# Kernel tuning notes

Measured on AMD Instinct MI355X. Metric: run time of the kernel, lower is better.

## Reference

```python
import jax, jax.numpy as jnp
import numpy as np

N_CHANNELS = 1024
N_HEADS = 16
BLOCK_SIZE = 2048
BATCH = 4
SEQ = 2048


def setup_inputs() -> dict:
    key = jax.random.key(0)
    k_x, k_wqkv, k_wproj = jax.random.split(key, 3)
    x = jax.random.normal(k_x, (BATCH, SEQ, N_CHANNELS), dtype=jnp.float32)
    # torch nn.Linear: y = x @ W.T + b, W shape [out, in], init normal(std=0.02)
    W_qkv = jax.random.normal(k_wqkv, (3 * N_CHANNELS, N_CHANNELS), dtype=jnp.float32) * 0.02
    b_qkv = jnp.zeros((3 * N_CHANNELS,), dtype=jnp.float32)
    W_proj = jax.random.normal(k_wproj, (N_CHANNELS, N_CHANNELS), dtype=jnp.float32) * 0.02
    b_proj = jnp.zeros((N_CHANNELS,), dtype=jnp.float32)
    return {"x": x, "W_qkv": W_qkv, "b_qkv": b_qkv, "W_proj": W_proj, "b_proj": b_proj}


def reference(x, W_qkv, b_qkv, W_proj, b_proj):
    bs, n, n_channels = x.shape
    n_heads = N_HEADS
    head_dim = n_channels // n_heads
    scale = head_dim ** (-0.5)

    qkv = x @ W_qkv.T + b_qkv                              # [b, n, 3C]
    qkv = qkv.reshape(bs, n, 3, n_heads, head_dim)
    q, k, v = qkv[:, :, 0], qkv[:, :, 1], qkv[:, :, 2]     # [b, n, h, d]

    logits = jnp.einsum('bthc,bshc->bhts', q, k) * scale   # [b, h, t, s]
    # causal mask: log(tril(ones)) = 0 below diagonal, -inf above
    causal = jnp.tril(jnp.ones((n, n), dtype=bool))
    logits = jnp.where(causal[None, None], logits, -jnp.inf)
    attn = jax.nn.softmax(logits, axis=-1)

    output = jnp.einsum('bhts,bshc->bthc', attn, v)        # [b, t, h, d]
    output = output.reshape(bs, n, n_channels)
    output = output @ W_proj.T + b_proj
    return output
```

## Files before the change

kernel.cpp:

```cpp
#include <hip/hip_runtime.h>
#include <hip/hip_bf16.h>
#include <stdint.h>

#define BATCH 4
#define SEQ   2048
#define NC    1024
#define NH    16
#define HD    64
#define NT    16

typedef __bf16 bf16x8 __attribute__((ext_vector_type(8)));
typedef __bf16 bf16x2 __attribute__((ext_vector_type(2)));
typedef float  f32x4  __attribute__((ext_vector_type(4)));
typedef float  f32x16 __attribute__((ext_vector_type(16)));

#define DEV __device__ __forceinline__

DEV unsigned short f2bf(float f) {
    union { float f; unsigned u; } v; v.f = f;
    unsigned r = (v.u + 0x7fffu + ((v.u >> 16) & 1u)) >> 16;
    return (unsigned short)r;
}

DEV float fast_exp2(float x) {
#if __has_builtin(__builtin_amdgcn_exp2f)
    return __builtin_amdgcn_exp2f(x);
#else
    return exp2f(x);
#endif
}

DEV void plane32_swap(uint32_t& a, uint32_t& b) {
#if __has_builtin(__builtin_amdgcn_permlane32_swap)
    auto r = __builtin_amdgcn_permlane32_swap(a, b, false, false);
    a = (uint32_t)r[0];
    b = (uint32_t)r[1];
#else
    uint32_t sa = __shfl_xor(a, 32), sb = __shfl_xor(b, 32);
    const bool hi = ((threadIdx.x & 63) >= 32);
    uint32_t na = hi ? sb : a;
    uint32_t nb = hi ? b : sa;
    a = na; b = nb;
#endif
}

#define GLDS16(gsrc, ldst)                                                           \
    __builtin_amdgcn_global_load_lds(                                                \
        (const __attribute__((address_space(1))) unsigned int*)(gsrc),               \
        (__attribute__((address_space(3))) unsigned int*)(ldst), 16, 0, 0)

#define CVT_N0 (BATCH * SEQ * NC / 4)
#define CVT_N1 (3 * NC * NC / 4)
#define CVT_N2 (NC * NC / 4)

__global__ void cvt_all_kernel(const float* __restrict__ x, unsigned short* __restrict__ xb,
                               const float* __restrict__ wq, unsigned short* __restrict__ wqb,
                               const float* __restrict__ wp, unsigned short* __restrict__ wpb) {
    int i = blockIdx.x * 256 + threadIdx.x;
    const float* src;
    unsigned short* dst;
    if (i < CVT_N0) {
        src = x; dst = xb;
    } else if (i < CVT_N0 + CVT_N1) {
        i -= CVT_N0; src = wq; dst = wqb;
    } else {
        i -= CVT_N0 + CVT_N1; src = wp; dst = wpb;
    }
    float4 v = reinterpret_cast<const float4*>(src)[i];
    ushort4 o;
    o.x = f2bf(v.x); o.y = f2bf(v.y); o.z = f2bf(v.z); o.w = f2bf(v.w);
    reinterpret_cast<ushort4*>(dst)[i] = o;
}

template <bool BF16_OUT>
__global__ __launch_bounds__(256, 2) void gemm_bt_kernel(
    const unsigned short* __restrict__ A,
    const unsigned short* __restrict__ W,
    const float* __restrict__ bias,
    void* __restrict__ Cout,
    int M, int N, int K, int scale_n, float scale)
{
    __shared__ __align__(16) char Alds[128 * 128];
    __shared__ __align__(16) char Blds[128 * 128];

    const int tid = threadIdx.x;
    const int w = tid >> 6, l = tid & 63, g = l >> 4, lr = l & 15;
    const int nt = N >> 7;
    const int cpx = gridDim.x >> 3;
    const int bid = (blockIdx.x & 7) * cpx + (blockIdx.x >> 3);
    const int mtile = bid / nt, ntile = bid % nt;
    const int m0 = mtile << 7, n0 = ntile << 7;
    const int wr = (w >> 1) << 6, wc = (w & 1) << 6;

    f32x4 acc[4][4] = {};

    for (int kt = 0; kt < K; kt += 64) {
        if (kt) __syncthreads();
#pragma unroll
        for (int i = 0; i < 4; ++i) {
            const int issue = (i << 2) + w;
            const int row = (issue << 3) + (l >> 3);
            const int chunk = (l & 7) ^ (row & 7);
            GLDS16((const char*)(A + (size_t)(m0 + row) * K + kt) + (chunk << 4),
                   Alds + (issue << 10));
        }
#pragma unroll
        for (int i = 0; i < 4; ++i) {
            const int issue = (i << 2) + w;
            const int row = (issue << 3) + (l >> 3);
            const int chunk = (l & 7) ^ (row & 7);
            GLDS16((const char*)(W + (size_t)(n0 + row) * K + kt) + (chunk << 4),
                   Blds + (issue << 10));
        }
        __syncthreads();

#pragma unroll
        for (int kb = 0; kb < 2; ++kb) {
            bf16x8 af[4], bfr[4];
#pragma unroll
            for (int mf = 0; mf < 4; ++mf) {
                const int row = wr + (mf << 4) + lr;
                const int chunk = ((kb << 2) + g) ^ (row & 7);
                af[mf] = *reinterpret_cast<const bf16x8*>(Alds + row * 128 + (chunk << 4));
            }
#pragma unroll
            for (int nf = 0; nf < 4; ++nf) {
                const int row = wc + (nf << 4) + lr;
                const int chunk = ((kb << 2) + g) ^ (row & 7);
                bfr[nf] = *reinterpret_cast<const bf16x8*>(Blds + row * 128 + (chunk << 4));
            }
#pragma unroll
            for (int mf = 0; mf < 4; ++mf)
#pragma unroll
                for (int nf = 0; nf < 4; ++nf)
                    acc[mf][nf] = __builtin_amdgcn_mfma_f32_16x16x32_bf16(
                        af[mf], bfr[nf], acc[mf][nf], 0, 0, 0);
        }
    }

#pragma unroll
    for (int mf = 0; mf < 4; ++mf) {
#pragma unroll
        for (int nf = 0; nf < 4; ++nf) {
            const int n = n0 + wc + (nf << 4) + lr;
            const float bscale = (n < scale_n) ? scale : 1.0f;
            const float bv = bias[n];
#pragma unroll
            for (int r = 0; r < 4; ++r) {
                const int m = m0 + wr + (mf << 4) + (g << 2) + r;
                float v2 = (acc[mf][nf][r] + bv) * bscale;
                if (BF16_OUT)
                    ((unsigned short*)Cout)[(size_t)m * N + n] = f2bf(v2);
                else
                    ((float*)Cout)[(size_t)m * N + n] = v2;
            }
        }
    }
}

__global__ __launch_bounds__(256, 2) void gemm_bt64_kernel(
    const unsigned short* __restrict__ A,
    const unsigned short* __restrict__ W,
    const float* __restrict__ bias,
    float* __restrict__ Cout,
    int M, int N, int K)
{
    __shared__ __align__(16) char Alds[64 * 128];
    __shared__ __align__(16) char Blds[128 * 128];

    const int tid = threadIdx.x;
    const int w = tid >> 6, l = tid & 63, g = l >> 4, lr = l & 15;
    const int nt = N >> 7;
    const int cpx = gridDim.x >> 3;
    const int bid = (blockIdx.x & 7) * cpx + (blockIdx.x >> 3);
    const int mtile = bid / nt, ntile = bid % nt;
    const int m0 = mtile << 6, n0 = ntile << 7;
    const int wr = (w >> 1) << 5, wc = (w & 1) << 6;

    f32x4 acc[2][4] = {};

    for (int kt = 0; kt < K; kt += 64) {
        if (kt) __syncthreads();
#pragma unroll
        for (int i = 0; i < 2; ++i) {
            const int issue = (i << 2) + w;
            const int row = (issue << 3) + (l >> 3);
            const int chunk = (l & 7) ^ (row & 7);
            GLDS16((const char*)(A + (size_t)(m0 + row) * K + kt) + (chunk << 4),
                   Alds + (issue << 10));
        }
#pragma unroll
        for (int i = 0; i < 4; ++i) {
            const int issue = (i << 2) + w;
            const int row = (issue << 3) + (l >> 3);
            const int chunk = (l & 7) ^ (row & 7);
            GLDS16((const char*)(W + (size_t)(n0 + row) * K + kt) + (chunk << 4),
                   Blds + (issue << 10));
        }
        __syncthreads();

#pragma unroll
        for (int kb = 0; kb < 2; ++kb) {
            bf16x8 af[2], bfr[4];
#pragma unroll
            for (int mf = 0; mf < 2; ++mf) {
                const int row = wr + (mf << 4) + lr;
                const int chunk = ((kb << 2) + g) ^ (row & 7);
                af[mf] = *reinterpret_cast<const bf16x8*>(Alds + row * 128 + (chunk << 4));
            }
#pragma unroll
            for (int nf = 0; nf < 4; ++nf) {
                const int row = wc + (nf << 4) + lr;
                const int chunk = ((kb << 2) + g) ^ (row & 7);
                bfr[nf] = *reinterpret_cast<const bf16x8*>(Blds + row * 128 + (chunk << 4));
            }
#pragma unroll
            for (int mf = 0; mf < 2; ++mf)
#pragma unroll
                for (int nf = 0; nf < 4; ++nf)
                    acc[mf][nf] = __builtin_amdgcn_mfma_f32_16x16x32_bf16(
                        af[mf], bfr[nf], acc[mf][nf], 0, 0, 0);
        }
    }

#pragma unroll
    for (int mf = 0; mf < 2; ++mf) {
#pragma unroll
        for (int nf = 0; nf < 4; ++nf) {
            const int n = n0 + wc + (nf << 4) + lr;
            const float bv = bias[n];
#pragma unroll
            for (int r = 0; r < 4; ++r) {
                const int m = m0 + wr + (mf << 4) + (g << 2) + r;
                Cout[(size_t)m * N + n] = acc[mf][nf][r] + bv;
            }
        }
    }
}

__global__ __launch_bounds__(256, 4) void attn_kernel(
    const unsigned short* __restrict__ qkv,
    unsigned short* __restrict__ ctx)
{
    __shared__ __align__(16) char Klds[2][8192];
    __shared__ __align__(16) char Vt[2][64 * 144];

    const int tid = threadIdx.x;
    const int w = tid >> 6, l = tid & 63, hi = l >> 5, lq = l & 31;
    const int bid = blockIdx.x;
    const int qt = NT - 1 - (bid >> 6);
    const int h = (bid >> 2) & 15, b = bid & 3;
    const unsigned short* base = qkv + (size_t)b * SEQ * 3072 + h * 64;

    const int vkey0 = (tid >> 5) << 3;
    const int vd0   = (tid & 31) << 1;
    const unsigned short* vbase = base + 2048 + (size_t)vkey0 * 3072 + vd0;

    const int q0 = (qt << 7) + (w << 5);
    const int q = q0 + lq;
    const int ntiles = (qt + 1) << 1;

    bf16x8 qfr[4];
#pragma unroll
    for (int ds = 0; ds < 4; ++ds)
        qfr[ds] = *reinterpret_cast<const bf16x8*>(
            base + (size_t)q * 3072 + (ds << 4) + (hi << 3));

    f32x16 acc0 = {}, acc1 = {};
    float lrun = 0.f;

    uint32_t vreg[8];

#pragma unroll
    for (int i = 0; i < 8; ++i)
        vreg[i] = *reinterpret_cast<const uint32_t*>(vbase + (size_t)i * 3072);
#pragma unroll
    for (int i = 0; i < 2; ++i) {
        const int issue = (i << 2) + w;
        const int row = (issue << 3) + (l >> 3);
        const int chunk = (l & 7) ^ (row & 7);
        GLDS16((const char*)(base + 1024 + (size_t)row * 3072) + (chunk << 4),
               Klds[0] + (issue << 10));
    }
    {
        uint4 a, bq;
        a.x = (vreg[0] & 0xffffu) | (vreg[1] << 16);
        a.y = (vreg[2] & 0xffffu) | (vreg[3] << 16);
        a.z = (vreg[4] & 0xffffu) | (vreg[5] << 16);
        a.w = (vreg[6] & 0xffffu) | (vreg[7] << 16);
        bq.x = (vreg[0] >> 16) | (vreg[1] & 0xffff0000u);
        bq.y = (vreg[2] >> 16) | (vreg[3] & 0xffff0000u);
        bq.z = (vreg[4] >> 16) | (vreg[5] & 0xffff0000u);
        bq.w = (vreg[6] >> 16) | (vreg[7] & 0xffff0000u);
        *reinterpret_cast<uint4*>(Vt[0] + vd0 * 144 + vkey0 * 2) = a;
        *reinterpret_cast<uint4*>(Vt[0] + (vd0 + 1) * 144 + vkey0 * 2) = bq;
    }
    __syncthreads();

    for (int t = 0; t < ntiles; ++t) {
        const int cur = t & 1;
        const int kv0 = t << 6;
        const bool pf_ = (t + 1 < ntiles);

        if (pf_) {
            const int kv1 = kv0 + 64;
#pragma unroll
            for (int i = 0; i < 8; ++i)
                vreg[i] = *reinterpret_cast<const uint32_t*>(
                    vbase + (size_t)(kv1 + i) * 3072);
#pragma unroll
            for (int i = 0; i < 2; ++i) {
                const int issue = (i << 2) + w;
                const int row = (issue << 3) + (l >> 3);
                const int chunk = (l & 7) ^ (row & 7);
                GLDS16((const char*)(base + 1024 + (size_t)(kv1 + row) * 3072) + (chunk << 4),
                       Klds[cur ^ 1] + (issue << 10));
            }
        }

        if (kv0 <= q0 + 31) {
            const bool do1 = (kv0 + 32 <= q0 + 31);

            f32x16 st0 = {}, st1 = {};
#pragma unroll
            for (int ds = 0; ds < 4; ++ds) {
                const int chunk = (((ds << 1) + hi) ^ (lq & 7)) << 4;
                bf16x8 k0 = *reinterpret_cast<const bf16x8*>(
                    Klds[cur] + lq * 128 + chunk);
                st0 = __builtin_amdgcn_mfma_f32_32x32x16_bf16(k0, qfr[ds], st0, 0, 0, 0);
            }
            if (do1) {
#pragma unroll
                for (int ds = 0; ds < 4; ++ds) {
                    const int chunk = (((ds << 1) + hi) ^ (lq & 7)) << 4;
                    bf16x8 k1 = *reinterpret_cast<const bf16x8*>(
                        Klds[cur] + (lq + 32) * 128 + chunk);
                    st1 = __builtin_amdgcn_mfma_f32_32x32x16_bf16(k1, qfr[ds], st1, 0, 0, 0);
                }
            }

            if (kv0 + 31 > q0) {
#pragma unroll
                for (int r = 0; r < 16; ++r) {
                    const int key = kv0 + ((r & 3) + ((r >> 2) << 3) + (hi << 2));
                    if (key > q) st0[r] = -INFINITY;
                }
            }
            if (do1 && kv0 + 63 > q0) {
#pragma unroll
                for (int r = 0; r < 16; ++r) {
                    const int key = kv0 + 32 + ((r & 3) + ((r >> 2) << 3) + (hi << 2));
                    if (key > q) st1[r] = -INFINITY;
                }
            }

            float rs = 0.f;
#pragma unroll
            for (int r = 0; r < 16; ++r) { st0[r] = fast_exp2(st0[r]); rs += st0[r]; }
            if (do1) {
#pragma unroll
                for (int r = 0; r < 16; ++r) { st1[r] = fast_exp2(st1[r]); rs += st1[r]; }
            }
            lrun += rs;

            uint32_t pk0[8], pk1[8];
#pragma unroll
            for (int sp = 0; sp < 4; ++sp)
#pragma unroll
                for (int c = 0; c < 2; ++c) {
                    bf16x2 t0 = {(__bf16)st0[(sp << 2) + (c << 1)],
                                 (__bf16)st0[(sp << 2) + (c << 1) + 1]};
                    pk0[(sp << 1) + c] = __builtin_bit_cast(uint32_t, t0);
                }
            if (do1) {
#pragma unroll
                for (int sp = 0; sp < 4; ++sp)
#pragma unroll
                    for (int c = 0; c < 2; ++c) {
                        bf16x2 t1 = {(__bf16)st1[(sp << 2) + (c << 1)],
                                     (__bf16)st1[(sp << 2) + (c << 1) + 1]};
                        pk1[(sp << 1) + c] = __builtin_bit_cast(uint32_t, t1);
                    }
            }

            const int nkt = do1 ? 4 : 2;
#pragma unroll
            for (int kt = 0; kt < 4; ++kt) {
                if (kt >= nkt) break;
                const int s0 = (kt & 1) << 1;
                uint32_t x0, x1, y0, y1;
                if (kt < 2) {
                    x0 = pk0[(s0 << 1) + 0]; x1 = pk0[(s0 << 1) + 1];
                    y0 = pk0[(s0 << 1) + 2]; y1 = pk0[(s0 << 1) + 3];
                } else {
                    x0 = pk1[(s0 << 1) + 0]; x1 = pk1[(s0 << 1) + 1];
                    y0 = pk1[(s0 << 1) + 2]; y1 = pk1[(s0 << 1) + 3];
                }
                plane32_swap(x0, y0);
                plane32_swap(x1, y1);
                union { uint32_t u[4]; bf16x8 v; } pf;
                pf.u[0] = x0; pf.u[1] = x1; pf.u[2] = y0; pf.u[3] = y1;

                const char* vrow = Vt[cur] + ((kt << 4) + (hi << 3)) * 2;
                bf16x8 vf0 = *reinterpret_cast<const bf16x8*>(vrow + lq * 144);
                bf16x8 vf1 = *reinterpret_cast<const bf16x8*>(vrow + (lq + 32) * 144);
                acc0 = __builtin_amdgcn_mfma_f32_32x32x16_bf16(vf0, pf.v, acc0, 0, 0, 0);
                acc1 = __builtin_amdgcn_mfma_f32_32x32x16_bf16(vf1, pf.v, acc1, 0, 0, 0);
            }
        }

        if (pf_) {
            uint4 a, bq;
            a.x = (vreg[0] & 0xffffu) | (vreg[1] << 16);
            a.y = (vreg[2] & 0xffffu) | (vreg[3] << 16);
            a.z = (vreg[4] & 0xffffu) | (vreg[5] << 16);
            a.w = (vreg[6] & 0xffffu) | (vreg[7] << 16);
            bq.x = (vreg[0] >> 16) | (vreg[1] & 0xffff0000u);
            bq.y = (vreg[2] >> 16) | (vreg[3] & 0xffff0000u);
            bq.z = (vreg[4] >> 16) | (vreg[5] & 0xffff0000u);
            bq.w = (vreg[6] >> 16) | (vreg[7] & 0xffff0000u);
            char* vt = Vt[cur ^ 1];
            *reinterpret_cast<uint4*>(vt + vd0 * 144 + vkey0 * 2) = a;
            *reinterpret_cast<uint4*>(vt + (vd0 + 1) * 144 + vkey0 * 2) = bq;
            __syncthreads();
        }
    }

    {
        const float ltot = lrun + __shfl_xor(lrun, 32);
        const float li = 1.0f / ltot;
        unsigned short* op = ctx + (size_t)(b * SEQ + q) * NC + h * HD;
#pragma unroll
        for (int grp = 0; grp < 4; ++grp) {
            ushort4 o0, o1;
            o0.x = f2bf(acc0[(grp << 2) + 0] * li);
            o0.y = f2bf(acc0[(grp << 2) + 1] * li);
            o0.z = f2bf(acc0[(grp << 2) + 2] * li);
            o0.w = f2bf(acc0[(grp << 2) + 3] * li);
            o1.x = f2bf(acc1[(grp << 2) + 0] * li);
            o1.y = f2bf(acc1[(grp << 2) + 1] * li);
            o1.z = f2bf(acc1[(grp << 2) + 2] * li);
            o1.w = f2bf(acc1[(grp << 2) + 3] * li);
            const int d = (grp << 3) + (hi << 2);
            *reinterpret_cast<ushort4*>(op + d) = o0;
            *reinterpret_cast<ushort4*>(op + d + 32) = o1;
        }
    }
}

extern "C" void kernel_launch(void* const* d_in, const int* in_sizes, int n_in,
                              void* d_out, int out_size, void* d_ws, size_t ws_size,
                              hipStream_t stream) {
    const float* x     = (const float*)d_in[0];
    const float* Wqkv  = (const float*)d_in[1];
    const float* bqkv  = (const float*)d_in[2];
    const float* Wproj = (const float*)d_in[3];
    const float* bproj = (const float*)d_in[4];
    float* out = (float*)d_out;

    const int M = BATCH * SEQ;
    unsigned short* ws = (unsigned short*)d_ws;
    unsigned short* xb     = ws;
    unsigned short* wqkvb  = xb + (size_t)M * NC;
    unsigned short* wprojb = wqkvb + (size_t)3 * NC * NC;
    unsigned short* qkvb   = wprojb + (size_t)NC * NC;
    unsigned short* ctxb   = qkvb + (size_t)M * 3 * NC;

    {
        const int total = CVT_N0 + CVT_N1 + CVT_N2;
        cvt_all_kernel<<<(total + 255) / 256, 256, 0, stream>>>(
            x, xb, Wqkv, wqkvb, Wproj, wprojb);
    }

    gemm_bt_kernel<true><<<(M / 128) * (3 * NC / 128), 256, 0, stream>>>(
        xb, wqkvb, bqkv, qkvb, M, 3 * NC, NC, NC, 0.18033688011112042f);

    attn_kernel<<<NT * NH * BATCH, 256, 0, stream>>>(qkvb, ctxb);

    gemm_bt64_kernel<<<(M / 64) * (NC / 128), 256, 0, stream>>>(
        ctxb, wprojb, bproj, out, M, NC, NC);
}
```

Before: 150.4 us.

## Split long causal query tiles into two KV halves with atomic-flag merge

The attention kernel now splits the work for the eight longest query tiles (qt>=8) into two blocks, each covering part of the KV range. A lookup schedule orders blocks so the heavy ones launch first. Each half writes its unnormalized fp32 partial output and row sums to scratch space, reusing the final output buffer. An atomic counter then lets the second finisher merge both halves and write the normalized bf16 context, aiming to balance load across CUs. This relies on the merge being valid without a running max, which the existing unnormalized accumulation seems to assume. It adds extra global traffic, fences, and a flag reset in the convert kernel.

Result: slower. 259.8 us (+72.8%).

```diff
diff --git a/kernel.cpp b/kernel.cpp
--- a/kernel.cpp
+++ b/kernel.cpp
@@ -49,13 +49,19 @@
         (const __attribute__((address_space(1))) unsigned int*)(gsrc),               \
         (__attribute__((address_space(3))) unsigned int*)(ldst), 16, 0, 0)
 
+__device__ const int QT_[24]  = {15,15, 7,14,14,13,13, 6,12,12,11,11, 5,10,10, 9, 9, 4, 8, 8, 3, 2, 1, 0};
+__device__ const int ST_[24]  = { 0,16, 0, 0,15, 0,14, 0, 0,13, 0,12, 0, 0,11, 0,10, 0, 0, 9, 0, 0, 0, 0};
+__device__ const int LEN_[24] = {16,16,16,15,15,14,14,14,13,13,12,12,12,11,11,10,10,10, 9, 9, 8, 6, 4, 2};
+
 #define CVT_N0 (BATCH * SEQ * NC / 4)
 #define CVT_N1 (3 * NC * NC / 4)
 #define CVT_N2 (NC * NC / 4)
 
 __global__ void cvt_all_kernel(const float* __restrict__ x, unsigned short* __restrict__ xb,
                                const float* __restrict__ wq, unsigned short* __restrict__ wqb,
-                               const float* __restrict__ wp, unsigned short* __restrict__ wpb) {
+                               const float* __restrict__ wp, unsigned short* __restrict__ wpb,
+                               unsigned int* __restrict__ flags) {
+    if (blockIdx.x < 2) flags[blockIdx.x * 256 + threadIdx.x] = 0;
     int i = blockIdx.x * 256 + threadIdx.x;
     const float* src;
     unsigned short* dst;
@@ -240,7 +246,10 @@
 
 __global__ __launch_bounds__(256, 4) void attn_kernel(
     const unsigned short* __restrict__ qkv,
-    unsigned short* __restrict__ ctx)
+    unsigned short* __restrict__ ctx,
+    float* __restrict__ opart,
+    float* __restrict__ lbuf,
+    unsigned int* __restrict__ flags)
 {
     __shared__ __align__(16) char Klds[2][8192];
     __shared__ __align__(16) char Vt[2][64 * 144];
@@ -248,8 +257,11 @@
     const int tid = threadIdx.x;
     const int w = tid >> 6, l = tid & 63, hi = l >> 5, lq = l & 31;
     const int bid = blockIdx.x;
-    const int qt = NT - 1 - (bid >> 6);
-    const int h = (bid >> 2) & 15, b = bid & 3;
+    const int type = bid >> 6;
+    const int hb = bid & 63;
+    const int qt = QT_[type], start = ST_[type], len = LEN_[type];
+    const int part = (qt >= 8) ? (start ? 1 : 0) : -1;
+    const int h = hb >> 2, b = hb & 3;
     const unsigned short* base = qkv + (size_t)b * SEQ * 3072 + h * 64;
 
     const int vkey0 = (tid >> 5) << 3;
@@ -258,7 +270,6 @@
 
     const int q0 = (qt << 7) + (w << 5);
     const int q = q0 + lq;
-    const int ntiles = (qt + 1) << 1;
 
     bf16x8 qfr[4];
 #pragma unroll
@@ -273,13 +284,14 @@
 
 #pragma unroll
     for (int i = 0; i < 8; ++i)
-        vreg[i] = *reinterpret_cast<const uint32_t*>(vbase + (size_t)i * 3072);
+        vreg[i] = *reinterpret_cast<const uint32_t*>(
+            vbase + (size_t)((start << 6) + i) * 3072);
 #pragma unroll
     for (int i = 0; i < 2; ++i) {
         const int issue = (i << 2) + w;
         const int row = (issue << 3) + (l >> 3);
         const int chunk = (l & 7) ^ (row & 7);
-        GLDS16((const char*)(base + 1024 + (size_t)row * 3072) + (chunk << 4),
+        GLDS16((const char*)(base + 1024 + (size_t)((start << 6) + row) * 3072) + (chunk << 4),
                Klds[0] + (issue << 10));
     }
     {
@@ -297,10 +309,10 @@
     }
     __syncthreads();
 
-    for (int t = 0; t < ntiles; ++t) {
-        const int cur = t & 1;
-        const int kv0 = t << 6;
-        const bool pf_ = (t + 1 < ntiles);
+    for (int tt = 0; tt < len; ++tt) {
+        const int cur = tt & 1;
+        const int kv0 = (start + tt) << 6;
+        const bool pf_ = (tt + 1 < len);
 
         if (pf_) {
             const int kv1 = kv0 + 64;
@@ -426,7 +438,7 @@
         }
     }
 
-    {
+    if (part < 0) {
         const float ltot = lrun + __shfl_xor(lrun, 32);
         const float li = 1.0f / ltot;
         unsigned short* op = ctx + (size_t)(b * SEQ + q) * NC + h * HD;
@@ -445,6 +457,66 @@
             *reinterpret_cast<ushort4*>(op + d) = o0;
             *reinterpret_cast<ushort4*>(op + d + 32) = o1;
         }
+        return;
+    }
+
+    const int pairid = ((qt - 8) << 6) + hb;
+    const int slot = (pairid << 1) + part;
+    float* op = opart + ((size_t)slot << 13) + (w << 11);
+#pragma unroll
+    for (int grp = 0; grp < 4; ++grp) {
+        f32x4 v0 = {acc0[(grp << 2) + 0], acc0[(grp << 2) + 1],
+                    acc0[(grp << 2) + 2], acc0[(grp << 2) + 3]};
+        *reinterpret_cast<f32x4*>(op + (grp << 8) + (l << 2)) = v0;
+        f32x4 v1 = {acc1[(grp << 2) + 0], acc1[(grp << 2) + 1],
+                    acc1[(grp << 2) + 2], acc1[(grp << 2) + 3]};
+        *reinterpret_cast<f32x4*>(op + 1024 + (grp << 8) + (l << 2)) = v1;
+    }
+    lbuf[(slot << 8) + (w << 6) + l] = lrun;
+
+    __syncthreads();
+    volatile unsigned* sflag = (volatile unsigned*)&Klds[0][0];
+    if (tid == 0) {
+        __threadfence();
+        *sflag = atomicAdd(&flags[pairid], 1u);
+    }
+    __syncthreads();
+    const unsigned old = *sflag;
+    if (old == 0) return;
+
+    __threadfence();
+    const int pslot = slot ^ 1;
+    const float* pp = opart + ((size_t)pslot << 13) + (w << 11);
+#pragma unroll
+    for (int grp = 0; grp < 4; ++grp) {
+        f32x4 v0 = *reinterpret_cast<const f32x4*>(pp + (grp << 8) + (l << 2));
+        f32x4 v1 = *reinterpret_cast<const f32x4*>(pp + 1024 + (grp << 8) + (l << 2));
+#pragma unroll
+        for (int j = 0; j < 4; ++j) {
+            acc0[(grp << 2) + j] += v0[j];
+            acc1[(grp << 2) + j] += v1[j];
+        }
+    }
+    lrun += lbuf[(pslot << 8) + (w << 6) + l];
+    {
+        const float ltot = lrun + __shfl_xor(lrun, 32);
+        const float li = 1.0f / ltot;
+        unsigned short* oc = ctx + (size_t)(b * SEQ + q) * NC + h * HD;
+#pragma unroll
+        for (int grp = 0; grp < 4; ++grp) {
+            ushort4 o0, o1;
+            o0.x = f2bf(acc0[(grp << 2) + 0] * li);
+            o0.y = f2bf(acc0[(grp << 2) + 1] * li);
+            o0.z = f2bf(acc0[(grp << 2) + 2] * li);
+            o0.w = f2bf(acc0[(grp << 2) + 3] * li);
+            o1.x = f2bf(acc1[(grp << 2) + 0] * li);
+            o1.y = f2bf(acc1[(grp << 2) + 1] * li);
+            o1.z = f2bf(acc1[(grp << 2) + 2] * li);
+            o1.w = f2bf(acc1[(grp << 2) + 3] * li);
+            const int d = (grp << 3) + (hi << 2);
+            *reinterpret_cast<ushort4*>(oc + d) = o0;
+            *reinterpret_cast<ushort4*>(oc + d + 32) = o1;
+        }
     }
 }
 
@@ -465,17 +537,19 @@
     unsigned short* wprojb = wqkvb + (size_t)3 * NC * NC;
     unsigned short* qkvb   = wprojb + (size_t)NC * NC;
     unsigned short* ctxb   = qkvb + (size_t)M * 3 * NC;
+    float* lbuf            = (float*)(ctxb + (size_t)M * NC);
+    unsigned int* flags    = (unsigned int*)(lbuf + 1024 * 256);
 
     {
         const int total = CVT_N0 + CVT_N1 + CVT_N2;
         cvt_all_kernel<<<(total + 255) / 256, 256, 0, stream>>>(
-            x, xb, Wqkv, wqkvb, Wproj, wprojb);
+            x, xb, Wqkv, wqkvb, Wproj, wprojb, flags);
     }
 
     gemm_bt_kernel<true><<<(M / 128) * (3 * NC / 128), 256, 0, stream>>>(
         xb, wqkvb, bqkv, qkvb, M, 3 * NC, NC, NC, 0.18033688011112042f);
 
-    attn_kernel<<<NT * NH * BATCH, 256, 0, stream>>>(qkvb, ctxb);
+    attn_kernel<<<24 * 64, 256, 0, stream>>>(qkvb, ctxb, out, lbuf, flags);
 
     gemm_bt64_kernel<<<(M / 64) * (NC / 128), 256, 0, stream>>>(
         ctxb, wprojb, bproj, out, M, NC, NC);
```

## Fuse x fp32-to-bf16 conversion into QKV GEMM A-tile loading

Applied to the files above, without the earlier changes.

The QKV projection GEMM now reads fp32 x directly, converts it to bf16 in registers and writes it to swizzled LDS. This replaces the separate conversion pass over x and its bf16 staging buffer. It removes a full read and write of the activation tensor. In exchange, each GEMM tile re-reads fp32 data at twice the bytes and routes A through registers instead of direct global-to-LDS loads.

After: 159.4 us. 1.06x slower.

```diff
diff --git a/kernel.cpp b/kernel.cpp
--- a/kernel.cpp
+++ b/kernel.cpp
@@ -49,22 +49,18 @@
         (const __attribute__((address_space(1))) unsigned int*)(gsrc),               \
         (__attribute__((address_space(3))) unsigned int*)(ldst), 16, 0, 0)
 
-#define CVT_N0 (BATCH * SEQ * NC / 4)
-#define CVT_N1 (3 * NC * NC / 4)
-#define CVT_N2 (NC * NC / 4)
-
-__global__ void cvt_all_kernel(const float* __restrict__ x, unsigned short* __restrict__ xb,
-                               const float* __restrict__ wq, unsigned short* __restrict__ wqb,
-                               const float* __restrict__ wp, unsigned short* __restrict__ wpb) {
+#define CVT_W1 (3 * NC * NC / 4)
+#define CVT_W2 (NC * NC / 4)
+
+__global__ void cvt_w_kernel(const float* __restrict__ wq, unsigned short* __restrict__ wqb,
+                             const float* __restrict__ wp, unsigned short* __restrict__ wpb) {
     int i = blockIdx.x * 256 + threadIdx.x;
     const float* src;
     unsigned short* dst;
-    if (i < CVT_N0) {
-        src = x; dst = xb;
-    } else if (i < CVT_N0 + CVT_N1) {
-        i -= CVT_N0; src = wq; dst = wqb;
+    if (i < CVT_W1) {
+        src = wq; dst = wqb;
     } else {
-        i -= CVT_N0 + CVT_N1; src = wp; dst = wpb;
+        i -= CVT_W1; src = wp; dst = wpb;
     }
     float4 v = reinterpret_cast<const float4*>(src)[i];
     ushort4 o;
@@ -72,12 +68,11 @@
     reinterpret_cast<ushort4*>(dst)[i] = o;
 }
 
-template <bool BF16_OUT>
-__global__ __launch_bounds__(256, 2) void gemm_bt_kernel(
-    const unsigned short* __restrict__ A,
+__global__ __launch_bounds__(256, 2) void gemm_xqkv_kernel(
+    const float* __restrict__ A,
     const unsigned short* __restrict__ W,
     const float* __restrict__ bias,
-    void* __restrict__ Cout,
+    unsigned short* __restrict__ Cout,
     int M, int N, int K, int scale_n, float scale)
 {
     __shared__ __align__(16) char Alds[128 * 128];
@@ -95,15 +90,16 @@
     f32x4 acc[4][4] = {};
 
     for (int kt = 0; kt < K; kt += 64) {
+        float4 a0[4], a1[4];
+#pragma unroll
+        for (int j = 0; j < 4; ++j) {
+            const int c = (j << 8) + tid;
+            const int row = c >> 3, cc = c & 7;
+            const float* src = A + (size_t)(m0 + row) * K + kt + (cc << 3);
+            a0[j] = *reinterpret_cast<const float4*>(src);
+            a1[j] = *reinterpret_cast<const float4*>(src + 4);
+        }
         if (kt) __syncthreads();
-#pragma unroll
-        for (int i = 0; i < 4; ++i) {
-            const int issue = (i << 2) + w;
-            const int row = (issue << 3) + (l >> 3);
-            const int chunk = (l & 7) ^ (row & 7);
-            GLDS16((const char*)(A + (size_t)(m0 + row) * K + kt) + (chunk << 4),
-                   Alds + (issue << 10));
-        }
 #pragma unroll
         for (int i = 0; i < 4; ++i) {
             const int issue = (i << 2) + w;
@@ -112,6 +108,14 @@
             GLDS16((const char*)(W + (size_t)(n0 + row) * K + kt) + (chunk << 4),
                    Blds + (issue << 10));
         }
+#pragma unroll
+        for (int j = 0; j < 4; ++j) {
+            const int c = (j << 8) + tid;
+            const int row = c >> 3, cc = c & 7;
+            bf16x8 v = {(__bf16)a0[j].x, (__bf16)a0[j].y, (__bf16)a0[j].z, (__bf16)a0[j].w,
+                        (__bf16)a1[j].x, (__bf16)a1[j].y, (__bf16)a1[j].z, (__bf16)a1[j].w};
+            *reinterpret_cast<bf16x8*>(Alds + row * 128 + ((cc ^ (row & 7)) << 4)) = v;
+        }
         __syncthreads();
 
 #pragma unroll
@@ -148,11 +152,7 @@
 #pragma unroll
             for (int r = 0; r < 4; ++r) {
                 const int m = m0 + wr + (mf << 4) + (g << 2) + r;
-                float v2 = (acc[mf][nf][r] + bv) * bscale;
-                if (BF16_OUT)
-                    ((unsigned short*)Cout)[(size_t)m * N + n] = f2bf(v2);
-                else
-                    ((float*)Cout)[(size_t)m * N + n] = v2;
+                Cout[(size_t)m * N + n] = f2bf((acc[mf][nf][r] + bv) * bscale);
             }
         }
     }
@@ -460,20 +460,19 @@
 
     const int M = BATCH * SEQ;
     unsigned short* ws = (unsigned short*)d_ws;
-    unsigned short* xb     = ws;
-    unsigned short* wqkvb  = xb + (size_t)M * NC;
+    unsigned short* wqkvb  = ws;
     unsigned short* wprojb = wqkvb + (size_t)3 * NC * NC;
     unsigned short* qkvb   = wprojb + (size_t)NC * NC;
     unsigned short* ctxb   = qkvb + (size_t)M * 3 * NC;
 
     {
-        const int total = CVT_N0 + CVT_N1 + CVT_N2;
-        cvt_all_kernel<<<(total + 255) / 256, 256, 0, stream>>>(
-            x, xb, Wqkv, wqkvb, Wproj, wprojb);
-    }
-
-    gemm_bt_kernel<true><<<(M / 128) * (3 * NC / 128), 256, 0, stream>>>(
-        xb, wqkvb, bqkv, qkvb, M, 3 * NC, NC, NC, 0.18033688011112042f);
+        const int total = CVT_W1 + CVT_W2;
+        cvt_w_kernel<<<(total + 255) / 256, 256, 0, stream>>>(
+            Wqkv, wqkvb, Wproj, wprojb);
+    }
+
+    gemm_xqkv_kernel<<<(M / 128) * (3 * NC / 128), 256, 0, stream>>>(
+        x, wqkvb, bqkv, qkvb, M, 3 * NC, NC, NC, 0.18033688011112042f);
 
     attn_kernel<<<NT * NH * BATCH, 256, 0, stream>>>(qkvb, ctxb);
 
```
